# Kernel tuning notes

Measured on AMD Instinct MI355X. Metric: run time of the kernel, lower is better.

The kernel has to match this reference:

```python
import jax, jax.numpy as jnp
import numpy as np

TAU = 0.08


def setup_inputs() -> dict:
    key = jax.random.key(0)
    k1, k2 = jax.random.split(key)
    pos_waves = jax.random.normal(k1, (32, 64, 8192), dtype=jnp.float32)
    neg_waves = jax.random.normal(k2, (32, 64, 8192), dtype=jnp.float32)
    return {"pos_waves": pos_waves, "neg_waves": neg_waves}


def _normalize(w):
    # global min/max over the whole wave tensor (matches torch.min/torch.max on 2D tensor)
    lo = jnp.min(w, axis=(1, 2), keepdims=True)  # [N,1,1]
    hi = jnp.max(w, axis=(1, 2), keepdims=True)
    return (w - lo) / (hi - lo)


def _pairwise_negpearson(X, Y):
    # X: [N,B,T], Y: [M,B,T] -> mean over B of (1 - pearson) for every (n,m) pair
    T = X.shape[-1]
    sx = jnp.sum(X, axis=-1)            # [N,B]
    sy = jnp.sum(Y, axis=-1)            # [M,B]
    sx2 = jnp.sum(X * X, axis=-1)       # [N,B]
    sy2 = jnp.sum(Y * Y, axis=-1)       # [M,B]
    sxy = jnp.einsum('nbt,mbt->nmb', X, Y)  # [N,M,B]
    num = T * sxy - sx[:, None, :] * sy[None, :, :]
    den = jnp.sqrt((T * sx2 - sx * sx)[:, None, :] * (T * sy2 - sy * sy)[None, :, :])
    return jnp.mean(1.0 - num / den, axis=-1)  # [N,M]


def reference(pos_waves, neg_waves):
    P = _normalize(pos_waves)   # [N,B,T]
    Q = _normalize(neg_waves)   # [M,B,T]
    N = P.shape[0]

    d_pp = _pairwise_negpearson(P, P)                    # [N,N]
    upper = jnp.triu(jnp.ones((N, N), dtype=bool), k=1)  # i < j pairs only
    pos_total = jnp.sum(jnp.where(upper, jnp.exp(d_pp / TAU), 0.0))

    d_pn = _pairwise_negpearson(P, Q)                    # [N,M]
    neg_total = jnp.sum(jnp.exp(d_pn / TAU))

    return jnp.log10(pos_total / neg_total + 1.0)
```

## Files before the change

kernel.cpp:

```cpp
#include <hip/hip_runtime.h>
#include <cmath>

#define N_ 32
#define B_ 64
#define T_ 8192
#define CPB 16
#define WAVES 4
#define TCHUNK (T_ / (CPB * WAVES))
#define KSTEPS (TCHUNK / 16)
#define PSTRIDE 2176

typedef _Float16 half8 __attribute__((ext_vector_type(8)));
typedef float floatx16 __attribute__((ext_vector_type(16)));

__global__ __launch_bounds__(256, 4) void k_stage1(const float* __restrict__ pos,
                                                   const float* __restrict__ neg,
                                                   float* __restrict__ partial) {
    __shared__ float lds_g[WAVES][2048];
    __shared__ float lds_s[WAVES][4][32];

    const int bid = blockIdx.x;
    const int b = bid >> 4, c = bid & 15;
    const int tid = threadIdx.x;
    const int w = tid >> 6, lane = tid & 63;
    const int r = lane & 31, h = lane >> 5;

    const long base = ((long)r * B_ + b) * T_;
    const int t0 = (c * WAVES + w) * TCHUNK + h * 8;
    const float4* px = (const float4*)(pos + base + t0);
    const float4* py = (const float4*)(neg + base + t0);

    floatx16 accpp = {};
    floatx16 accpn = {};
    float sx = 0.f, sx2 = 0.f, sy = 0.f, sy2 = 0.f;

#pragma unroll
    for (int s = 0; s < KSTEPS; ++s) {
        float4 xa = px[s * 4 + 0];
        float4 xb = px[s * 4 + 1];
        float4 ya = py[s * 4 + 0];
        float4 yb = py[s * 4 + 1];

        half8 xf, yf;
        xf[0] = (_Float16)xa.x; xf[1] = (_Float16)xa.y;
        xf[2] = (_Float16)xa.z; xf[3] = (_Float16)xa.w;
        xf[4] = (_Float16)xb.x; xf[5] = (_Float16)xb.y;
        xf[6] = (_Float16)xb.z; xf[7] = (_Float16)xb.w;
        yf[0] = (_Float16)ya.x; yf[1] = (_Float16)ya.y;
        yf[2] = (_Float16)ya.z; yf[3] = (_Float16)ya.w;
        yf[4] = (_Float16)yb.x; yf[5] = (_Float16)yb.y;
        yf[6] = (_Float16)yb.z; yf[7] = (_Float16)yb.w;

        accpp = __builtin_amdgcn_mfma_f32_32x32x16_f16(xf, xf, accpp, 0, 0, 0);
        accpn = __builtin_amdgcn_mfma_f32_32x32x16_f16(xf, yf, accpn, 0, 0, 0);

        sx += xa.x + xa.y + xa.z + xa.w + xb.x + xb.y + xb.z + xb.w;
        sy += ya.x + ya.y + ya.z + ya.w + yb.x + yb.y + yb.z + yb.w;
        sx2 = fmaf(xa.x, xa.x, sx2); sx2 = fmaf(xa.y, xa.y, sx2);
        sx2 = fmaf(xa.z, xa.z, sx2); sx2 = fmaf(xa.w, xa.w, sx2);
        sx2 = fmaf(xb.x, xb.x, sx2); sx2 = fmaf(xb.y, xb.y, sx2);
        sx2 = fmaf(xb.z, xb.z, sx2); sx2 = fmaf(xb.w, xb.w, sx2);
        sy2 = fmaf(ya.x, ya.x, sy2); sy2 = fmaf(ya.y, ya.y, sy2);
        sy2 = fmaf(ya.z, ya.z, sy2); sy2 = fmaf(ya.w, ya.w, sy2);
        sy2 = fmaf(yb.x, yb.x, sy2); sy2 = fmaf(yb.y, yb.y, sy2);
        sy2 = fmaf(yb.z, yb.z, sy2); sy2 = fmaf(yb.w, yb.w, sy2);
    }

    sx += __shfl_xor(sx, 32);
    sx2 += __shfl_xor(sx2, 32);
    sy += __shfl_xor(sy, 32);
    sy2 += __shfl_xor(sy2, 32);

#pragma unroll
    for (int reg = 0; reg < 16; ++reg) {
        int row = (reg & 3) + 8 * (reg >> 2) + 4 * h;
        lds_g[w][row * 32 + r] = accpp[reg];
        lds_g[w][1024 + row * 32 + r] = accpn[reg];
    }
    if (lane < 32) {
        lds_s[w][0][r] = sx;
        lds_s[w][1][r] = sx2;
        lds_s[w][2][r] = sy;
        lds_s[w][3][r] = sy2;
    }
    __syncthreads();

    float* out = partial + (long)bid * PSTRIDE;
    for (int o = tid; o < 2048; o += 256)
        out[o] = lds_g[0][o] + lds_g[1][o] + lds_g[2][o] + lds_g[3][o];
    if (tid < 128) {
        int kind = tid >> 5, row = tid & 31;
        out[2048 + tid] = lds_s[0][kind][row] + lds_s[1][kind][row] +
                          lds_s[2][kind][row] + lds_s[3][kind][row];
    }
}

__global__ void k_reduce(const float* __restrict__ partial, float* __restrict__ red) {
    const int b = blockIdx.x;
    const float* in = partial + (long)b * CPB * PSTRIDE;
    float* out = red + (long)b * PSTRIDE;
    for (int o = threadIdx.x; o < PSTRIDE; o += blockDim.x) {
        float s = 0.f;
#pragma unroll
        for (int c = 0; c < CPB; ++c) s += in[c * PSTRIDE + o];
        out[o] = s;
    }
}

__global__ void k_entries(const float* __restrict__ red, double* __restrict__ blocksums) {
    const int tid = threadIdx.x;
    const int w = tid >> 6, lane = tid & 63;
    const int entry = blockIdx.x * 4 + w;
    const int mat = entry >> 10;
    const int idx = entry & 1023;
    const int n = idx >> 5, m = idx & 31;

    const float* rb = red + (long)lane * PSTRIDE;
    float g = rb[mat * 1024 + idx];
    float sxn = rb[2048 + n];
    float sx2n = rb[2080 + n];
    float sym, sy2m;
    if (mat == 0) {
        sym = rb[2048 + m];
        sy2m = rb[2080 + m];
    } else {
        sym = rb[2112 + m];
        sy2m = rb[2144 + m];
    }

    double num = (double)T_ * (double)g - (double)sxn * (double)sym;
    double vx = (double)T_ * (double)sx2n - (double)sxn * (double)sxn;
    double vy = (double)T_ * (double)sy2m - (double)sym * (double)sym;
    double contrib = 1.0 - num / sqrt(vx * vy);

#pragma unroll
    for (int off = 32; off; off >>= 1) contrib += __shfl_down(contrib, off);

    __shared__ double s_pos[4], s_neg[4];
    if (lane == 0) {
        double d = contrib * (1.0 / B_);
        double term = exp(d / 0.08);
        double p = 0.0, q = 0.0;
        if (mat == 0) {
            if (n < m) p = term;
        } else {
            q = term;
        }
        s_pos[w] = p;
        s_neg[w] = q;
    }
    __syncthreads();
    if (tid == 0) {
        blocksums[blockIdx.x * 2 + 0] = s_pos[0] + s_pos[1] + s_pos[2] + s_pos[3];
        blocksums[blockIdx.x * 2 + 1] = s_neg[0] + s_neg[1] + s_neg[2] + s_neg[3];
    }
}

__global__ void k_final(const double* __restrict__ blocksums, float* __restrict__ out) {
    __shared__ double sp[256], sn[256];
    const int tid = threadIdx.x;
    double p = 0.0, q = 0.0;
    for (int i = tid; i < 512; i += 256) {
        p += blocksums[2 * i + 0];
        q += blocksums[2 * i + 1];
    }
    sp[tid] = p;
    sn[tid] = q;
    __syncthreads();
    for (int s = 128; s; s >>= 1) {
        if (tid < s) {
            sp[tid] += sp[tid + s];
            sn[tid] += sn[tid + s];
        }
        __syncthreads();
    }
    if (tid == 0) out[0] = (float)log10(sp[0] / sn[0] + 1.0);
}

extern "C" void kernel_launch(void* const* d_in, const int* in_sizes, int n_in,
                              void* d_out, int out_size, void* d_ws, size_t ws_size,
                              hipStream_t stream) {
    const float* pos = (const float*)d_in[0];
    const float* neg = (const float*)d_in[1];
    float* out = (float*)d_out;

    char* ws = (char*)d_ws;
    float* partial = (float*)ws;
    float* red = (float*)(ws + (size_t)1024 * PSTRIDE * 4);
    double* blocksums = (double*)(ws + (size_t)1024 * PSTRIDE * 4 + (size_t)64 * PSTRIDE * 4);

    k_stage1<<<1024, 256, 0, stream>>>(pos, neg, partial);
    k_reduce<<<64, 256, 0, stream>>>(partial, red);
    k_entries<<<512, 256, 0, stream>>>(red, blocksums);
    k_final<<<1, 256, 0, stream>>>(blocksums, out);
}
```

Measured before the change: 184.1 us.

## Stage stage1 inputs through LDS with coalesced row loads, widen reduce grid

```diff
diff --git a/kernel.cpp b/kernel.cpp
--- a/kernel.cpp
+++ b/kernel.cpp
@@ -5,106 +5,98 @@
 #define B_ 64
 #define T_ 8192
 #define CPB 16
-#define WAVES 4
-#define TCHUNK (T_ / (CPB * WAVES))
-#define KSTEPS (TCHUNK / 16)
 #define PSTRIDE 2176
+#define PADH 264
 
+typedef _Float16 half4 __attribute__((ext_vector_type(4)));
 typedef _Float16 half8 __attribute__((ext_vector_type(8)));
 typedef float floatx16 __attribute__((ext_vector_type(16)));
 
 __global__ __launch_bounds__(256, 4) void k_stage1(const float* __restrict__ pos,
                                                    const float* __restrict__ neg,
                                                    float* __restrict__ partial) {
-    __shared__ float lds_g[WAVES][2048];
-    __shared__ float lds_s[WAVES][4][32];
+    __shared__ __align__(16) char smem[2 * 32 * PADH * 2];
+    _Float16(*tile)[32][PADH] = (_Float16(*)[32][PADH])smem;
+    float* scratch = (float*)smem;
 
     const int bid = blockIdx.x;
     const int b = bid >> 4, c = bid & 15;
     const int tid = threadIdx.x;
     const int w = tid >> 6, lane = tid & 63;
-    const int r = lane & 31, h = lane >> 5;
+    const int row = tid >> 3;
+    const int oct = tid & 7;
+    const int m = lane & 31, h = lane >> 5;
 
-    const long base = ((long)r * B_ + b) * T_;
-    const int t0 = (c * WAVES + w) * TCHUNK + h * 8;
-    const float4* px = (const float4*)(pos + base + t0);
-    const float4* py = (const float4*)(neg + base + t0);
+    const float* xrow = pos + ((long)row * B_ + b) * T_ + c * 512;
+    const float* yrow = neg + ((long)row * B_ + b) * T_ + c * 512;
 
     floatx16 accpp = {};
     floatx16 accpn = {};
     float sx = 0.f, sx2 = 0.f, sy = 0.f, sy2 = 0.f;
 
 #pragma unroll
-    for (int s = 0; s < KSTEPS; ++s) {
-        float4 xa = px[s * 4 + 0];
-        float4 xb = px[s * 4 + 1];
-        float4 ya = py[s * 4 + 0];
-        float4 yb = py[s * 4 + 1];
+    for (int s = 0; s < 2; ++s) {
+        __syncthreads();
+        const float4* px = (const float4*)(xrow + s * 256);
+        const float4* py = (const float4*)(yrow + s * 256);
+#pragma unroll
+        for (int f = 0; f < 8; ++f) {
+            float4 v = px[f * 8 + oct];
+            sx += v.x + v.y + v.z + v.w;
+            sx2 = fmaf(v.x, v.x, sx2); sx2 = fmaf(v.y, v.y, sx2);
+            sx2 = fmaf(v.z, v.z, sx2); sx2 = fmaf(v.w, v.w, sx2);
+            half4 hv = {(_Float16)v.x, (_Float16)v.y, (_Float16)v.z, (_Float16)v.w};
+            *(half4*)&tile[0][row][f * 32 + oct * 4] = hv;
 
-        half8 xf, yf;
-        xf[0] = (_Float16)xa.x; xf[1] = (_Float16)xa.y;
-        xf[2] = (_Float16)xa.z; xf[3] = (_Float16)xa.w;
-        xf[4] = (_Float16)xb.x; xf[5] = (_Float16)xb.y;
-        xf[6] = (_Float16)xb.z; xf[7] = (_Float16)xb.w;
-        yf[0] = (_Float16)ya.x; yf[1] = (_Float16)ya.y;
-        yf[2] = (_Float16)ya.z; yf[3] = (_Float16)ya.w;
-        yf[4] = (_Float16)yb.x; yf[5] = (_Float16)yb.y;
-        yf[6] = (_Float16)yb.z; yf[7] = (_Float16)yb.w;
-
-        accpp = __builtin_amdgcn_mfma_f32_32x32x16_f16(xf, xf, accpp, 0, 0, 0);
-        accpn = __builtin_amdgcn_mfma_f32_32x32x16_f16(xf, yf, accpn, 0, 0, 0);
-
-        sx += xa.x + xa.y + xa.z + xa.w + xb.x + xb.y + xb.z + xb.w;
-        sy += ya.x + ya.y + ya.z + ya.w + yb.x + yb.y + yb.z + yb.w;
-        sx2 = fmaf(xa.x, xa.x, sx2); sx2 = fmaf(xa.y, xa.y, sx2);
-        sx2 = fmaf(xa.z, xa.z, sx2); sx2 = fmaf(xa.w, xa.w, sx2);
-        sx2 = fmaf(xb.x, xb.x, sx2); sx2 = fmaf(xb.y, xb.y, sx2);
-        sx2 = fmaf(xb.z, xb.z, sx2); sx2 = fmaf(xb.w, xb.w, sx2);
-        sy2 = fmaf(ya.x, ya.x, sy2); sy2 = fmaf(ya.y, ya.y, sy2);
-        sy2 = fmaf(ya.z, ya.z, sy2); sy2 = fmaf(ya.w, ya.w, sy2);
-        sy2 = fmaf(yb.x, yb.x, sy2); sy2 = fmaf(yb.y, yb.y, sy2);
-        sy2 = fmaf(yb.z, yb.z, sy2); sy2 = fmaf(yb.w, yb.w, sy2);
+            float4 u = py[f * 8 + oct];
+            sy += u.x + u.y + u.z + u.w;
+            sy2 = fmaf(u.x, u.x, sy2); sy2 = fmaf(u.y, u.y, sy2);
+            sy2 = fmaf(u.z, u.z, sy2); sy2 = fmaf(u.w, u.w, sy2);
+            half4 hu = {(_Float16)u.x, (_Float16)u.y, (_Float16)u.z, (_Float16)u.w};
+            *(half4*)&tile[1][row][f * 32 + oct * 4] = hu;
+        }
+        __syncthreads();
+#pragma unroll
+        for (int kk = 0; kk < 4; ++kk) {
+            const int t0 = w * 64 + kk * 16 + h * 8;
+            half8 xf = *(const half8*)&tile[0][m][t0];
+            half8 yf = *(const half8*)&tile[1][m][t0];
+            accpp = __builtin_amdgcn_mfma_f32_32x32x16_f16(xf, xf, accpp, 0, 0, 0);
+            accpn = __builtin_amdgcn_mfma_f32_32x32x16_f16(xf, yf, accpn, 0, 0, 0);
+        }
     }
 
-    sx += __shfl_xor(sx, 32);
-    sx2 += __shfl_xor(sx2, 32);
-    sy += __shfl_xor(sy, 32);
-    sy2 += __shfl_xor(sy2, 32);
+    sx += __shfl_xor(sx, 1); sx += __shfl_xor(sx, 2); sx += __shfl_xor(sx, 4);
+    sx2 += __shfl_xor(sx2, 1); sx2 += __shfl_xor(sx2, 2); sx2 += __shfl_xor(sx2, 4);
+    sy += __shfl_xor(sy, 1); sy += __shfl_xor(sy, 2); sy += __shfl_xor(sy, 4);
+    sy2 += __shfl_xor(sy2, 1); sy2 += __shfl_xor(sy2, 2); sy2 += __shfl_xor(sy2, 4);
 
+    float* out = partial + (long)bid * PSTRIDE;
+    if (oct < 4) {
+        float v = (oct == 0) ? sx : (oct == 1) ? sx2 : (oct == 2) ? sy : sy2;
+        out[2048 + oct * 32 + row] = v;
+    }
+
+    __syncthreads();
 #pragma unroll
     for (int reg = 0; reg < 16; ++reg) {
-        int row = (reg & 3) + 8 * (reg >> 2) + 4 * h;
-        lds_g[w][row * 32 + r] = accpp[reg];
-        lds_g[w][1024 + row * 32 + r] = accpn[reg];
-    }
-    if (lane < 32) {
-        lds_s[w][0][r] = sx;
-        lds_s[w][1][r] = sx2;
-        lds_s[w][2][r] = sy;
-        lds_s[w][3][r] = sy2;
+        int rr = (reg & 3) + 8 * (reg >> 2) + 4 * h;
+        scratch[w * 2048 + rr * 32 + m] = accpp[reg];
+        scratch[w * 2048 + 1024 + rr * 32 + m] = accpn[reg];
     }
     __syncthreads();
-
-    float* out = partial + (long)bid * PSTRIDE;
     for (int o = tid; o < 2048; o += 256)
-        out[o] = lds_g[0][o] + lds_g[1][o] + lds_g[2][o] + lds_g[3][o];
-    if (tid < 128) {
-        int kind = tid >> 5, row = tid & 31;
-        out[2048 + tid] = lds_s[0][kind][row] + lds_s[1][kind][row] +
-                          lds_s[2][kind][row] + lds_s[3][kind][row];
-    }
+        out[o] = scratch[o] + scratch[2048 + o] + scratch[4096 + o] + scratch[6144 + o];
 }
 
 __global__ void k_reduce(const float* __restrict__ partial, float* __restrict__ red) {
-    const int b = blockIdx.x;
+    const int b = blockIdx.y;
+    const int o = blockIdx.x * 128 + threadIdx.x;
     const float* in = partial + (long)b * CPB * PSTRIDE;
-    float* out = red + (long)b * PSTRIDE;
-    for (int o = threadIdx.x; o < PSTRIDE; o += blockDim.x) {
-        float s = 0.f;
+    float s = 0.f;
 #pragma unroll
-        for (int c = 0; c < CPB; ++c) s += in[c * PSTRIDE + o];
-        out[o] = s;
-    }
+    for (int c = 0; c < CPB; ++c) s += in[c * PSTRIDE + o];
+    red[(long)b * PSTRIDE + o] = s;
 }
 
 __global__ void k_entries(const float* __restrict__ red, double* __restrict__ blocksums) {
@@ -190,7 +182,7 @@
     double* blocksums = (double*)(ws + (size_t)1024 * PSTRIDE * 4 + (size_t)64 * PSTRIDE * 4);
 
     k_stage1<<<1024, 256, 0, stream>>>(pos, neg, partial);
-    k_reduce<<<64, 256, 0, stream>>>(partial, red);
+    k_reduce<<<dim3(17, 64), 128, 0, stream>>>(partial, red);
     k_entries<<<512, 256, 0, stream>>>(red, blocksums);
     k_final<<<1, 256, 0, stream>>>(blocksums, out);
 }
```

After: 156.8 us. -14.8%, faster.
